# Kernel optimization log

Measured on AMD Instinct MI355X. Metric: run time of the kernel, lower is better.

Reference implementation:

```python
import jax, jax.numpy as jnp
import numpy as np

N_NODES = 100000
N_EDGES = 1600000
IN_G = 128
IN_R = 64
HID = 128
N_GRAPHS = 512
BN_EPS = 1e-5


def _gcn_conv(x, W, b, src, dst, norm, n_nodes):
    # PyG GCNConv: h = X W; out[i] = sum_j norm_ij * h[j] over edges (incl. self-loops); + bias
    h = x @ W  # [N, C]
    msgs = h[src] * norm[:, None]  # [E', C]
    agg = jax.ops.segment_sum(msgs, dst, num_segments=n_nodes)
    return agg + b


def setup_inputs() -> dict:
    key = jax.random.key(0)
    ks = jax.random.split(key, 12)
    x = jax.random.normal(ks[0], (N_NODES, IN_G), dtype=jnp.float32)
    edge_index = jax.random.randint(ks[1], (2, N_EDGES), 0, N_NODES, dtype=jnp.int64)
    batch = jnp.sort(jax.random.randint(ks[2], (N_NODES,), 0, N_GRAPHS, dtype=jnp.int64))
    rst = jax.random.normal(ks[3], (N_GRAPHS, IN_R), dtype=jnp.float32)

    def lin(k, fan_in, fan_out):
        bound = 1.0 / np.sqrt(fan_in)
        k1, k2 = jax.random.split(k)
        W = jax.random.uniform(k1, (fan_in, fan_out), minval=-bound, maxval=bound, dtype=jnp.float32)
        b = jax.random.uniform(k2, (fan_out,), minval=-bound, maxval=bound, dtype=jnp.float32)
        return W, b

    W1, b1 = lin(ks[4], IN_G, HID)
    W2, b2 = lin(ks[5], HID, HID)
    Wg, bg = lin(ks[6], HID, HID // 2)
    Wr, br = lin(ks[7], IN_R, HID // 2)
    Wc, bc = lin(ks[8], HID, 2)
    gamma = jnp.ones((HID,), dtype=jnp.float32)
    beta = jnp.zeros((HID,), dtype=jnp.float32)
    return {"x": x, "edge_index": edge_index, "batch": batch, "rst": rst,
            "num_graphs": N_GRAPHS,
            "W1": W1, "b1": b1, "gamma": gamma, "beta": beta,
            "W2": W2, "b2": b2, "Wg": Wg, "bg": bg,
            "Wr": Wr, "br": br, "Wc": Wc, "bc": bc}


def reference(x, edge_index, batch, rst, num_graphs,
              W1, b1, gamma, beta, W2, b2, Wg, bg, Wr, br, Wc, bc):
    n = x.shape[0]
    # add self-loops (PyG GCNConv default)
    loop = jnp.arange(n, dtype=edge_index.dtype)
    src = jnp.concatenate([edge_index[0], loop])
    dst = jnp.concatenate([edge_index[1], loop])
    deg = jax.ops.segment_sum(jnp.ones_like(dst, dtype=x.dtype), dst, num_segments=n)
    dinv = jnp.where(deg > 0, jax.lax.rsqrt(deg), 0.0)
    norm = dinv[src] * dinv[dst]  # [E+N]

    h = _gcn_conv(x, W1, b1, src, dst, norm, n)
    # BatchNorm1d with batch statistics (training math; dropout omitted / eval)
    mu = jnp.mean(h, axis=0)
    var = jnp.var(h, axis=0)
    h = gamma * (h - mu) * jax.lax.rsqrt(var + BN_EPS) + beta
    h = jax.nn.relu(h)
    h = _gcn_conv(h, W2, b2, src, dst, norm, n)

    # global mean pool
    sums = jax.ops.segment_sum(h, batch, num_segments=num_graphs)
    counts = jax.ops.segment_sum(jnp.ones((n,), dtype=h.dtype), batch, num_segments=num_graphs)
    pooled = sums / jnp.maximum(counts, 1.0)[:, None]  # [G, HID]

    x_graph = jax.nn.relu(pooled @ Wg + bg)
    x_rst = jax.nn.relu(rst @ Wr + br)
    x_comb = jnp.concatenate([x_graph, x_rst], axis=1)
    return x_comb @ Wc + bc
```

## Files before the change

kernel.cpp:

```cpp
#include <hip/hip_runtime.h>


typedef __attribute__((ext_vector_type(8))) short bf16x8;
typedef __attribute__((ext_vector_type(4))) float f32x4;
typedef __attribute__((ext_vector_type(2))) float f32x2;
typedef __attribute__((ext_vector_type(2))) unsigned u32x2;
typedef __attribute__((ext_vector_type(4))) unsigned u32x4;

#define NBKT_MAX 256
#define BKT_SHIFT 9
#define TILE_E 2000
#define BSORT_CAP 4096

__device__ __forceinline__ float bf_lo(unsigned u) {
  union { unsigned u; float f; } c; c.u = u << 16; return c.f;
}
__device__ __forceinline__ float bf_hi(unsigned u) {
  union { unsigned u; float f; } c; c.u = u & 0xffff0000u; return c.f;
}
__device__ __forceinline__ unsigned short f32_bf16(float f) {
  union { float f; unsigned u; } c; c.f = f;
  return (unsigned short)((c.u + 0x7fffu + ((c.u >> 16) & 1u)) >> 16);
}
__device__ __forceinline__ unsigned pack_bf16(float a, float b) {
  return (unsigned)f32_bf16(a) | ((unsigned)f32_bf16(b) << 16);
}
__device__ __forceinline__ unsigned pack_fp8x4(float c0, float c1, float c2, float c3) {
  int w = __builtin_amdgcn_cvt_pk_fp8_f32(c0, c1, 0, false);
  w = __builtin_amdgcn_cvt_pk_fp8_f32(c2, c3, w, true);
  return (unsigned)w;
}
__device__ __forceinline__ int aload(int* p) { return atomicAdd(p, 0); }

__global__ __launch_bounds__(256) void tile_hist_kernel(const int* __restrict__ dst,
                                                        int* __restrict__ tcnt,
                                                        int* __restrict__ counts,
                                                        float* __restrict__ stats,
                                                        const int* __restrict__ batch,
                                                        int* __restrict__ gstart,
                                                        int* __restrict__ syncp,
                                                        int e, int ntiles, int nbkt,
                                                        int n, int G) {
  __shared__ int hist[NBKT_MAX];
  int tile = blockIdx.x, tid = threadIdx.x;
  int idx = blockIdx.x * 256 + tid;
  if (idx < n) counts[idx] = 1;
  if (idx < 256) stats[idx] = 0.f;
  if (idx < 8) syncp[idx] = 0;
  if (idx <= G) {
    int g = idx;
    if (g == G) gstart[g] = n;
    else {
      int lo = 0, hi = n;
      while (lo < hi) {
        int mid = (lo + hi) >> 1;
        if (batch[mid] < g) lo = mid + 1; else hi = mid;
      }
      gstart[g] = lo;
    }
  }
  for (int b = tid; b < nbkt; b += 256) hist[b] = 0;
  __syncthreads();
  int t0 = tile * TILE_E;
  int tend = t0 + TILE_E; if (tend > e) tend = e;
  for (int i = t0 + tid; i < tend; i += 256)
    atomicAdd(&hist[__builtin_nontemporal_load(&dst[i]) >> BKT_SHIFT], 1);
  __syncthreads();
  for (int b = tid; b < nbkt; b += 256) tcnt[b * ntiles + tile] = hist[b];
}

__global__ __launch_bounds__(1024) void scan_ticket_kernel(const int* __restrict__ src,
                                                           int* __restrict__ dst,
                                                           int* __restrict__ bsum,
                                                           int* __restrict__ boff,
                                                           int* __restrict__ syncp,
                                                           float* __restrict__ dinv,
                                                           int n, int nb) {
  __shared__ int wsum[16];
  __shared__ int sflag, soff;
  int tid = threadIdx.x, lane = tid & 63, wid = tid >> 6;
  int bid = blockIdx.x;
  int idx = bid * 1024 + tid;
  int orig = (idx < n) ? src[idx] : 0;
  if (dinv != nullptr && idx < n) dinv[idx] = rsqrtf((float)orig);
  int v = orig;
#pragma unroll
  for (int d = 1; d < 64; d <<= 1) {
    int t = __shfl_up(v, d, 64);
    if (lane >= d) v += t;
  }
  if (lane == 63) wsum[wid] = v;
  __syncthreads();
  if (wid == 0 && lane < 16) {
    int s = wsum[lane];
#pragma unroll
    for (int d = 1; d < 16; d <<= 1) {
      int t = __shfl_up(s, d, 64);
      if (lane >= d) s += t;
    }
    wsum[lane] = s;
  }
  __syncthreads();
  int wexcl = (wid == 0) ? 0 : wsum[wid - 1];
  int lexcl = wexcl + (v - orig);
  if (tid == 0) {
    atomicExch(&bsum[bid], wsum[15]);
    __threadfence();
    int t = atomicAdd(&syncp[0], 1);
    sflag = (t == nb - 1) ? 1 : 0;
  }
  __syncthreads();
  if (sflag) {
    if (tid < 64) {
      int base = tid * 4;
      int a0 = (base + 0 < nb) ? aload(&bsum[base + 0]) : 0;
      int a1 = (base + 1 < nb) ? aload(&bsum[base + 1]) : 0;
      int a2 = (base + 2 < nb) ? aload(&bsum[base + 2]) : 0;
      int a3 = (base + 3 < nb) ? aload(&bsum[base + 3]) : 0;
      int local = a0 + a1 + a2 + a3, s = local;
#pragma unroll
      for (int d = 1; d < 64; d <<= 1) {
        int t = __shfl_up(s, d, 64);
        if (tid >= d) s += t;
      }
      int excl = s - local;
      if (base + 0 < nb) atomicExch(&boff[base + 0], excl);
      if (base + 1 < nb) atomicExch(&boff[base + 1], excl + a0);
      if (base + 2 < nb) atomicExch(&boff[base + 2], excl + a0 + a1);
      if (base + 3 < nb) atomicExch(&boff[base + 3], excl + a0 + a1 + a2);
      __threadfence();
    }
    __syncthreads();
    if (tid == 0) atomicExch(&syncp[1], 1);
  }
  if (tid == 0) {
    while (aload(&syncp[1]) == 0) __builtin_amdgcn_s_sleep(8);
    soff = aload(&boff[bid]);
  }
  __syncthreads();
  if (idx < n) dst[idx] = soff + lexcl;
}

__global__ __launch_bounds__(256) void tile_scatter_kernel(const int* __restrict__ src,
                                                           const int* __restrict__ dst,
                                                           const int* __restrict__ tcnt,
                                                           const int* __restrict__ toff,
                                                           int2* __restrict__ pedge,
                                                           int e, int ntiles, int nbkt) {
  __shared__ int hb[NBKT_MAX], cnt[NBKT_MAX], gbase[NBKT_MAX];
  __shared__ int2 led[TILE_E];
  int tile = blockIdx.x, tid = threadIdx.x;
  for (int b = tid; b < nbkt; b += 256) {
    hb[b] = tcnt[b * ntiles + tile];
    gbase[b] = toff[b * ntiles + tile];
    cnt[b] = 0;
  }
  __syncthreads();
  if (tid < 64) {
    int b4 = tid * 4;
    int h0 = (b4 + 0 < nbkt) ? hb[b4 + 0] : 0;
    int h1 = (b4 + 1 < nbkt) ? hb[b4 + 1] : 0;
    int h2 = (b4 + 2 < nbkt) ? hb[b4 + 2] : 0;
    int h3 = (b4 + 3 < nbkt) ? hb[b4 + 3] : 0;
    int local = h0 + h1 + h2 + h3, v = local;
#pragma unroll
    for (int d = 1; d < 64; d <<= 1) {
      int t = __shfl_up(v, d, 64);
      if (tid >= d) v += t;
    }
    int excl = v - local;
    if (b4 + 0 < nbkt) hb[b4 + 0] = excl;
    if (b4 + 1 < nbkt) hb[b4 + 1] = excl + h0;
    if (b4 + 2 < nbkt) hb[b4 + 2] = excl + h0 + h1;
    if (b4 + 3 < nbkt) hb[b4 + 3] = excl + h0 + h1 + h2;
  }
  __syncthreads();
  int t0 = tile * TILE_E;
  int tend = t0 + TILE_E; if (tend > e) tend = e;
  for (int i = t0 + tid; i < tend; i += 256) {
    int s = __builtin_nontemporal_load(&src[i]);
    int d = __builtin_nontemporal_load(&dst[i]);
    int bkt = d >> BKT_SHIFT;
    int slot = hb[bkt] + atomicAdd(&cnt[bkt], 1);
    led[slot] = make_int2(s, d);
  }
  __syncthreads();
  int tc = tend - t0;
  for (int j = tid; j < tc; j += 256) {
    int2 sd = led[j];
    int bkt = sd.y >> BKT_SHIFT;
    pedge[gbase[bkt] + (j - hb[bkt])] = sd;
  }
}

__global__ __launch_bounds__(256) void deg_count_kernel(const int2* __restrict__ pedge,
                                                        const int* __restrict__ toff,
                                                        int* __restrict__ counts,
                                                        int e, int ntiles, int nbkt, int n) {
  __shared__ int cnt[512];
  int b = blockIdx.x >> 2, qu = blockIdx.x & 3;
  int nb0 = b << BKT_SHIFT;
  int nn = n - nb0; if (nn > 512) nn = 512;
  for (int l = threadIdx.x; l < 512; l += 256) cnt[l] = 0;
  __syncthreads();
  int estart = toff[b * ntiles];
  int eend = (b + 1 < nbkt) ? toff[(b + 1) * ntiles] : e;
  int len = eend - estart;
  int qb = estart + (int)((long long)len * qu / 4);
  int qe = estart + (int)((long long)len * (qu + 1) / 4);
  for (int i = qb + threadIdx.x; i < qe; i += 256)
    atomicAdd(&cnt[pedge[i].y - nb0], 1);
  __syncthreads();
  for (int l = threadIdx.x; l < nn; l += 256) {
    int c = cnt[l];
    if (c) atomicAdd(&counts[nb0 + l], c);
  }
}

__global__ __launch_bounds__(256) void bucket_sort_kernel(const int2* __restrict__ pedge,
                                                          const int* __restrict__ toff,
                                                          const int* __restrict__ cursor,
                                                          int* __restrict__ sorted_src,
                                                          int e, int etot,
                                                          int ntiles, int nbkt, int n) {
  __shared__ int lcur[128];
  __shared__ int lsrc[BSORT_CAP];
  int b = blockIdx.x >> 2, qu = blockIdx.x & 3;
  int nb0 = b << BKT_SHIFT;
  int q0 = nb0 + qu * 128;
  if (q0 >= n) return;
  int q1 = q0 + 128; if (q1 > n) q1 = n;
  int qn = q1 - q0;
  int estart = toff[b * ntiles];
  int eend = (b + 1 < nbkt) ? toff[(b + 1) * ntiles] : e;
  int qstart = cursor[q0];
  int qend = (q1 < n) ? cursor[q1] : etot;
  for (int l = threadIdx.x; l < qn; l += 256) lcur[l] = cursor[q0 + l] - qstart;
  __syncthreads();
  for (int i = estart + threadIdx.x; i < eend; i += 256) {
    int2 sd = pedge[i];
    unsigned rel = (unsigned)(sd.y - q0);
    if (rel < (unsigned)qn) {
      int pos = atomicAdd(&lcur[rel], 1);
      if (pos < BSORT_CAP) lsrc[pos] = sd.x;
    }
  }
  __syncthreads();
  for (int l = threadIdx.x; l < qn; l += 256) {
    int pos = lcur[l];
    if (pos < BSORT_CAP) lsrc[pos] = q0 + l;
  }
  __syncthreads();
  int qc = qend - qstart; if (qc > BSORT_CAP) qc = BSORT_CAP;
  for (int j = threadIdx.x; j < qc; j += 256) sorted_src[qstart + j] = lsrc[j];
}

template <int MODE>
__global__ __launch_bounds__(256) void gemm_mfma_kernel(const void* __restrict__ Ap,
                                                        const float* __restrict__ W,
                                                        const float* __restrict__ dinv,
                                                        const float* __restrict__ stats,
                                                        const float* __restrict__ gamma,
                                                        const float* __restrict__ beta,
                                                        unsigned* __restrict__ Cb, int n) {
  __shared__ unsigned short WB[16384];
  __shared__ float scs[128], shs[128];
  int tid = threadIdx.x;
  if (MODE == 1 && tid < 128) {
    float invN = 1.f / (float)n;
    float mu = stats[tid] * invN;
    float var = stats[128 + tid] * invN - mu * mu;
    float rstd = rsqrtf(var + 1e-5f);
    float s = gamma[tid] * rstd;
    scs[tid] = s;
    shs[tid] = beta[tid] - mu * s;
  }
  for (int t = tid; t < 2048; t += 256) {
    int nl = t & 15, ct = (t >> 4) & 7, qq = (t >> 7) & 3, kt = t >> 9;
    int c = ct * 16 + nl;
    int k0 = kt * 32 + qq * 8;
    union { bf16x8 v; unsigned short s[8]; } u;
#pragma unroll
    for (int j = 0; j < 8; ++j) u.s[j] = f32_bf16(W[(k0 + j) * 128 + c]);
    *(bf16x8*)&WB[(size_t)t * 8] = u.v;
  }
  __syncthreads();
  int lane = tid & 63;
  int m = lane & 15, q = lane >> 4;
  float scr[4][8], shr[4][8];
  if (MODE == 1) {
#pragma unroll
    for (int kt = 0; kt < 4; ++kt)
#pragma unroll
      for (int j = 0; j < 8; ++j) {
        int c = kt * 32 + q * 8 + j;
        scr[kt][j] = scs[c];
        shr[kt][j] = shs[c];
      }
  }
  int wv = (int)((blockIdx.x * 256u + tid) >> 6);
  int nwv = (int)((gridDim.x * 256u) >> 6);
  int ntl = n >> 4;
  for (int t = wv; t < ntl; t += nwv) {
    int row = t * 16 + m;
    bf16x8 af[4];
    if (MODE == 1) {
      const u32x4* Au = (const u32x4*)((const unsigned*)Ap + (size_t)row * 64 + q * 4);
#pragma unroll
      for (int kt = 0; kt < 4; ++kt) {
        u32x4 w = Au[kt * 4];
        float y0 = fmaxf(fmaf(scr[kt][0], bf_lo(w.x), shr[kt][0]), 0.f);
        float y1 = fmaxf(fmaf(scr[kt][1], bf_hi(w.x), shr[kt][1]), 0.f);
        float y2 = fmaxf(fmaf(scr[kt][2], bf_lo(w.y), shr[kt][2]), 0.f);
        float y3 = fmaxf(fmaf(scr[kt][3], bf_hi(w.y), shr[kt][3]), 0.f);
        float y4 = fmaxf(fmaf(scr[kt][4], bf_lo(w.z), shr[kt][4]), 0.f);
        float y5 = fmaxf(fmaf(scr[kt][5], bf_hi(w.z), shr[kt][5]), 0.f);
        float y6 = fmaxf(fmaf(scr[kt][6], bf_lo(w.w), shr[kt][6]), 0.f);
        float y7 = fmaxf(fmaf(scr[kt][7], bf_hi(w.w), shr[kt][7]), 0.f);
        union { bf16x8 v; unsigned uu[4]; } uf;
        uf.uu[0] = pack_bf16(y0, y1);
        uf.uu[1] = pack_bf16(y2, y3);
        uf.uu[2] = pack_bf16(y4, y5);
        uf.uu[3] = pack_bf16(y6, y7);
        af[kt] = uf.v;
      }
    } else {
      const float* Arow = (const float*)Ap + (size_t)row * 128 + q * 8;
#pragma unroll
      for (int kt = 0; kt < 4; ++kt) {
        f32x4 a0 = *(const f32x4*)(Arow + kt * 32);
        f32x4 a1 = *(const f32x4*)(Arow + kt * 32 + 4);
        union { bf16x8 v; unsigned short s[8]; } u;
        u.s[0] = f32_bf16(a0.x); u.s[1] = f32_bf16(a0.y);
        u.s[2] = f32_bf16(a0.z); u.s[3] = f32_bf16(a0.w);
        u.s[4] = f32_bf16(a1.x); u.s[5] = f32_bf16(a1.y);
        u.s[6] = f32_bf16(a1.z); u.s[7] = f32_bf16(a1.w);
        af[kt] = u.v;
      }
    }
    f32x4 acc[8];
#pragma unroll
    for (int ct = 0; ct < 8; ++ct) acc[ct] = (f32x4){0.f, 0.f, 0.f, 0.f};
#pragma unroll
    for (int kt = 0; kt < 4; ++kt) {
#pragma unroll
      for (int ct = 0; ct < 8; ++ct) {
        bf16x8 b = *(const bf16x8*)&WB[(((kt * 4 + q) * 8 + ct) * 16 + m) * 8];
        acc[ct] = __builtin_amdgcn_mfma_f32_16x16x32_bf16(b, af[kt], acc[ct], 0, 0, 0);
      }
    }
    float dv = dinv[row];
#pragma unroll
    for (int ct = 0; ct < 8; ++ct) {
      unsigned wout = pack_fp8x4(acc[ct][0] * dv, acc[ct][1] * dv,
                                 acc[ct][2] * dv, acc[ct][3] * dv);
      Cb[(size_t)row * 32 + ct * 4 + q] = wout;
    }
  }
}

__global__ __launch_bounds__(256) void gather_kernel(const unsigned* __restrict__ g,
    const int* __restrict__ srcs, const int* __restrict__ cursor,
    const int* __restrict__ counts, const float* __restrict__ dinv,
    unsigned* __restrict__ out, int n) {
  int lane = threadIdx.x & 63;
  int grp = lane >> 4;
  int sub = lane & 15;
  int gw = (int)((blockIdx.x * blockDim.x + threadIdx.x) >> 6);
  int nw = (int)((gridDim.x * blockDim.x) >> 6);
  for (int i0 = gw; i0 < n; i0 += nw) {
    int i = __builtin_amdgcn_readfirstlane(i0);
    int beg = cursor[i];
    int cnt2 = counts[i];
    float di = dinv[i];
    f32x2 A0 = {0.f, 0.f}, A1 = {0.f, 0.f}, A2 = {0.f, 0.f}, A3 = {0.f, 0.f};
#define ACC8(W0, W1)                                                       \
    { A0 += __builtin_amdgcn_cvt_pk_f32_fp8((int)(W0), false);             \
      A1 += __builtin_amdgcn_cvt_pk_f32_fp8((int)(W0), true);              \
      A2 += __builtin_amdgcn_cvt_pk_f32_fp8((int)(W1), false);             \
      A3 += __builtin_amdgcn_cvt_pk_f32_fp8((int)(W1), true); }
    int e = 0;
    for (; e + 16 <= cnt2; e += 16) {
      int sA = srcs[beg + e + grp];
      int sB = srcs[beg + e + grp + 4];
      int sC = srcs[beg + e + grp + 8];
      int sD = srcs[beg + e + grp + 12];
      u32x2 vA = *((const u32x2*)(g + ((size_t)sA << 5)) + sub);
      u32x2 vB = *((const u32x2*)(g + ((size_t)sB << 5)) + sub);
      u32x2 vC = *((const u32x2*)(g + ((size_t)sC << 5)) + sub);
      u32x2 vD = *((const u32x2*)(g + ((size_t)sD << 5)) + sub);
      ACC8(vA.x, vA.y) ACC8(vB.x, vB.y) ACC8(vC.x, vC.y) ACC8(vD.x, vD.y)
    }
    for (; e + 4 <= cnt2; e += 4) {
      int s = srcs[beg + e + grp];
      u32x2 v = *((const u32x2*)(g + ((size_t)s << 5)) + sub);
      ACC8(v.x, v.y)
    }
    if (e < cnt2) {
      int k = e + grp;
      int kk = (k < cnt2) ? k : cnt2 - 1;
      int s = srcs[beg + kk];
      float sel = (k < cnt2) ? 1.f : 0.f;
      u32x2 v = *((const u32x2*)(g + ((size_t)s << 5)) + sub);
      f32x2 p0 = __builtin_amdgcn_cvt_pk_f32_fp8((int)v.x, false);
      f32x2 p1 = __builtin_amdgcn_cvt_pk_f32_fp8((int)v.x, true);
      f32x2 p2 = __builtin_amdgcn_cvt_pk_f32_fp8((int)v.y, false);
      f32x2 p3 = __builtin_amdgcn_cvt_pk_f32_fp8((int)v.y, true);
      A0 += p0 * sel; A1 += p1 * sel; A2 += p2 * sel; A3 += p3 * sel;
    }
#undef ACC8
    float a0 = A0.x, a1 = A0.y, a2 = A1.x, a3 = A1.y;
    float a4 = A2.x, a5 = A2.y, a6 = A3.x, a7 = A3.y;
    a0 += __shfl_xor(a0, 16, 64); a0 += __shfl_xor(a0, 32, 64);
    a1 += __shfl_xor(a1, 16, 64); a1 += __shfl_xor(a1, 32, 64);
    a2 += __shfl_xor(a2, 16, 64); a2 += __shfl_xor(a2, 32, 64);
    a3 += __shfl_xor(a3, 16, 64); a3 += __shfl_xor(a3, 32, 64);
    a4 += __shfl_xor(a4, 16, 64); a4 += __shfl_xor(a4, 32, 64);
    a5 += __shfl_xor(a5, 16, 64); a5 += __shfl_xor(a5, 32, 64);
    a6 += __shfl_xor(a6, 16, 64); a6 += __shfl_xor(a6, 32, 64);
    a7 += __shfl_xor(a7, 16, 64); a7 += __shfl_xor(a7, 32, 64);
    if (grp == 0) {
      u32x4 o;
      o.x = pack_bf16(di * a0, di * a1);
      o.y = pack_bf16(di * a2, di * a3);
      o.z = pack_bf16(di * a4, di * a5);
      o.w = pack_bf16(di * a6, di * a7);
      *((u32x4*)(out + ((size_t)i << 6)) + sub) = o;
    }
  }
}

__global__ __launch_bounds__(256) void bn_stats_kernel(const unsigned* __restrict__ a,
                                                       float* __restrict__ stats, int n) {
  int c2 = threadIdx.x & 63;
  int ph = threadIdx.x >> 6;
  float s0 = 0.f, s1 = 0.f, q0 = 0.f, q1 = 0.f;
  for (int r = blockIdx.x * 4 + ph; r < n; r += gridDim.x * 4) {
    unsigned v = a[(size_t)r * 64 + c2];
    float x0 = bf_lo(v), x1 = bf_hi(v);
    s0 += x0; s1 += x1; q0 += x0 * x0; q1 += x1 * x1;
  }
  __shared__ float ls[4][64][4];
  ls[ph][c2][0] = s0; ls[ph][c2][1] = s1; ls[ph][c2][2] = q0; ls[ph][c2][3] = q1;
  __syncthreads();
  if (threadIdx.x < 64) {
    int c = threadIdx.x;
    float S0 = 0.f, S1 = 0.f, Q0 = 0.f, Q1 = 0.f;
#pragma unroll
    for (int p = 0; p < 4; ++p) {
      S0 += ls[p][c][0]; S1 += ls[p][c][1]; Q0 += ls[p][c][2]; Q1 += ls[p][c][3];
    }
    atomicAdd(&stats[2 * c], S0);
    atomicAdd(&stats[2 * c + 1], S1);
    atomicAdd(&stats[128 + 2 * c], Q0);
    atomicAdd(&stats[129 + 2 * c], Q1);
  }
}

__global__ __launch_bounds__(256) void poolhead_kernel(const unsigned* __restrict__ a,
    const int* __restrict__ gstart, const float* __restrict__ b2,
    const float* __restrict__ rst, const float* __restrict__ Wg,
    const float* __restrict__ bg, const float* __restrict__ Wr,
    const float* __restrict__ br, const float* __restrict__ Wc,
    const float* __restrict__ bc, float* __restrict__ out, int G) {
  int g = blockIdx.x;
  int t = threadIdx.x;
  int c2 = t & 63;
  int ph = t >> 6;
  int s = gstart[g], e = gstart[g + 1];
  float a0 = 0.f, a1 = 0.f;
  for (int r = s + ph; r < e; r += 4) {
    unsigned v = a[(size_t)r * 64 + c2];
    a0 += bf_lo(v); a1 += bf_hi(v);
  }
  __shared__ float ls[4][64][2];
  __shared__ float xp[128];
  __shared__ float xc[128];
  ls[ph][c2][0] = a0; ls[ph][c2][1] = a1;
  __syncthreads();
  if (t < 64) {
    int c = t;
    float S0 = 0.f, S1 = 0.f;
#pragma unroll
    for (int p = 0; p < 4; ++p) { S0 += ls[p][c][0]; S1 += ls[p][c][1]; }
    int cnt = e - s;
    float inv = (cnt > 0) ? 1.f / (float)cnt : 0.f;
    xp[2 * c]     = (cnt > 0) ? (S0 * inv + b2[2 * c]) : 0.f;
    xp[2 * c + 1] = (cnt > 0) ? (S1 * inv + b2[2 * c + 1]) : 0.f;
  }
  __syncthreads();
  if (t < 64) {
    float acc = bg[t];
    for (int k = 0; k < 128; ++k) acc = fmaf(xp[k], Wg[k * 64 + t], acc);
    xc[t] = fmaxf(acc, 0.f);
  } else if (t < 128) {
    int j = t - 64;
    float acc = br[j];
    const float* __restrict__ r = rst + (size_t)g * 64;
    for (int k = 0; k < 64; ++k) acc = fmaf(r[k], Wr[k * 64 + j], acc);
    xc[t] = fmaxf(acc, 0.f);
  }
  __syncthreads();
  if (t < 2) {
    float acc = bc[t];
    for (int j = 0; j < 128; ++j) acc = fmaf(xc[j], Wc[j * 2 + t], acc);
    out[(size_t)g * 2 + t] = acc;
  }
}

extern "C" void kernel_launch(void* const* d_in, const int* in_sizes, int n_in,
                              void* d_out, int out_size, void* d_ws, size_t ws_size,
                              hipStream_t stream) {
  (void)n_in; (void)ws_size;
  const float* x     = (const float*)d_in[0];
  const int*   ei    = (const int*)d_in[1];
  const int*   batch = (const int*)d_in[2];
  const float* rst   = (const float*)d_in[3];
  const float* W1    = (const float*)d_in[5];
  const float* gamma = (const float*)d_in[7];
  const float* beta  = (const float*)d_in[8];
  const float* W2    = (const float*)d_in[9];
  const float* b2    = (const float*)d_in[10];
  const float* Wg    = (const float*)d_in[11];
  const float* bg    = (const float*)d_in[12];
  const float* Wr    = (const float*)d_in[13];
  const float* br    = (const float*)d_in[14];
  const float* Wc    = (const float*)d_in[15];
  const float* bc    = (const float*)d_in[16];
  float* out = (float*)d_out;

  int N = in_sizes[0] / 128;
  int E = in_sizes[1] / 2;
  int G = out_size / 2;
  int ETOT = E + N;
  const int* esrc = ei;
  const int* edst = ei + E;

  int nbkt = (N + 511) >> BKT_SHIFT;
  int ntiles = (E + TILE_E - 1) / TILE_E;
  int tlen = nbkt * ntiles;

  char* ws = (char*)d_ws;
  size_t off = 0;
  auto alloc = [&](size_t bytes) -> void* {
    void* p = ws + off;
    off += (bytes + 255) & ~(size_t)255;
    return p;
  };
  unsigned* hb  = (unsigned*)alloc((size_t)N * 32 * 4);
  unsigned* agb = (unsigned*)alloc((size_t)N * 64 * 4);
  int* sorted   = (int*)alloc((size_t)ETOT * 4 + 256);
  int2* pedge   = (int2*)alloc((size_t)E * 8);
  int* tcnt     = (int*)alloc((size_t)tlen * 4);
  int* toff     = (int*)alloc((size_t)tlen * 4);
  int* counts   = (int*)alloc((size_t)N * 4);
  int* cursor   = (int*)alloc((size_t)N * 4);
  float* dinv   = (float*)alloc((size_t)N * 4);
  float* stats  = (float*)alloc(256 * 4);
  int* gstart   = (int*)alloc((size_t)(G + 1) * 4);
  int* bsum     = (int*)alloc(256 * 4);
  int* boff     = (int*)alloc(256 * 4);
  int* syncp    = (int*)alloc(8 * 4);

  int nscan = (N + 1023) / 1024;
  int ntscan = (tlen + 1023) / 1024;
  int gblocks = (N / 16 + 3) / 4;

  tile_hist_kernel<<<ntiles, 256, 0, stream>>>(edst, tcnt, counts, stats, batch,
                                               gstart, syncp, E, ntiles, nbkt, N, G);
  scan_ticket_kernel<<<ntscan, 1024, 0, stream>>>(tcnt, toff, bsum, boff,
                                                  syncp, nullptr, tlen, ntscan);
  tile_scatter_kernel<<<ntiles, 256, 0, stream>>>(esrc, edst, tcnt, toff, pedge, E, ntiles, nbkt);
  deg_count_kernel<<<nbkt * 4, 256, 0, stream>>>(pedge, toff, counts, E, ntiles, nbkt, N);
  scan_ticket_kernel<<<nscan, 1024, 0, stream>>>(counts, cursor, bsum, boff,
                                                 syncp + 2, dinv, N, nscan);
  bucket_sort_kernel<<<nbkt * 4, 256, 0, stream>>>(pedge, toff, cursor, sorted,
                                                   E, ETOT, ntiles, nbkt, N);

  gemm_mfma_kernel<0><<<gblocks, 256, 0, stream>>>(x, W1, dinv, stats, gamma, beta, hb, N);
  gather_kernel<<<4096, 256, 0, stream>>>(hb, sorted, cursor, counts, dinv, agb, N);

  bn_stats_kernel<<<512, 256, 0, stream>>>(agb, stats, N);

  gemm_mfma_kernel<1><<<gblocks, 256, 0, stream>>>(agb, W2, dinv, stats, gamma, beta, hb, N);
  gather_kernel<<<4096, 256, 0, stream>>>(hb, sorted, cursor, counts, dinv, agb, N);

  poolhead_kernel<<<G, 256, 0, stream>>>(agb, gstart, b2, rst, Wg, bg, Wr, br,
                                         Wc, bc, out, G);
}
```

Measured before the change: 375.6 us.

## Fold degree counting into scatter and prefetch next tile in GEMM

```diff
diff --git a/kernel.cpp b/kernel.cpp
--- a/kernel.cpp
+++ b/kernel.cpp
@@ -44,7 +44,7 @@
   __shared__ int hist[NBKT_MAX];
   int tile = blockIdx.x, tid = threadIdx.x;
   int idx = blockIdx.x * 256 + tid;
-  if (idx < n) counts[idx] = 1;
+  if (idx < n) counts[idx] = 0;
   if (idx < 256) stats[idx] = 0.f;
   if (idx < 8) syncp[idx] = 0;
   if (idx <= G) {
@@ -75,13 +75,13 @@
                                                            int* __restrict__ boff,
                                                            int* __restrict__ syncp,
                                                            float* __restrict__ dinv,
-                                                           int n, int nb) {
+                                                           int n, int nb, int addone) {
   __shared__ int wsum[16];
   __shared__ int sflag, soff;
   int tid = threadIdx.x, lane = tid & 63, wid = tid >> 6;
   int bid = blockIdx.x;
   int idx = bid * 1024 + tid;
-  int orig = (idx < n) ? src[idx] : 0;
+  int orig = (idx < n) ? (src[idx] + addone) : 0;
   if (dinv != nullptr && idx < n) dinv[idx] = rsqrtf((float)orig);
   int v = orig;
 #pragma unroll
@@ -146,6 +146,7 @@
                                                            const int* __restrict__ tcnt,
                                                            const int* __restrict__ toff,
                                                            int2* __restrict__ pedge,
+                                                           int* __restrict__ counts,
                                                            int e, int ntiles, int nbkt) {
   __shared__ int hb[NBKT_MAX], cnt[NBKT_MAX], gbase[NBKT_MAX];
   __shared__ int2 led[TILE_E];
@@ -183,6 +184,7 @@
     int bkt = d >> BKT_SHIFT;
     int slot = hb[bkt] + atomicAdd(&cnt[bkt], 1);
     led[slot] = make_int2(s, d);
+    atomicAdd(&counts[d], 1);
   }
   __syncthreads();
   int tc = tend - t0;
@@ -190,30 +192,6 @@
     int2 sd = led[j];
     int bkt = sd.y >> BKT_SHIFT;
     pedge[gbase[bkt] + (j - hb[bkt])] = sd;
-  }
-}
-
-__global__ __launch_bounds__(256) void deg_count_kernel(const int2* __restrict__ pedge,
-                                                        const int* __restrict__ toff,
-                                                        int* __restrict__ counts,
-                                                        int e, int ntiles, int nbkt, int n) {
-  __shared__ int cnt[512];
-  int b = blockIdx.x >> 2, qu = blockIdx.x & 3;
-  int nb0 = b << BKT_SHIFT;
-  int nn = n - nb0; if (nn > 512) nn = 512;
-  for (int l = threadIdx.x; l < 512; l += 256) cnt[l] = 0;
-  __syncthreads();
-  int estart = toff[b * ntiles];
-  int eend = (b + 1 < nbkt) ? toff[(b + 1) * ntiles] : e;
-  int len = eend - estart;
-  int qb = estart + (int)((long long)len * qu / 4);
-  int qe = estart + (int)((long long)len * (qu + 1) / 4);
-  for (int i = qb + threadIdx.x; i < qe; i += 256)
-    atomicAdd(&cnt[pedge[i].y - nb0], 1);
-  __syncthreads();
-  for (int l = threadIdx.x; l < nn; l += 256) {
-    int c = cnt[l];
-    if (c) atomicAdd(&counts[nb0 + l], c);
   }
 }
 
@@ -301,14 +279,45 @@
   int wv = (int)((blockIdx.x * 256u + tid) >> 6);
   int nwv = (int)((gridDim.x * 256u) >> 6);
   int ntl = n >> 4;
+  if (wv >= ntl) return;
+  f32x4 cf0, cf1, cf2, cf3, cf4, cf5, cf6, cf7;
+  u32x4 cu0, cu1, cu2, cu3;
+  {
+    int row = wv * 16 + m;
+    if (MODE == 1) {
+      const u32x4* Au = (const u32x4*)((const unsigned*)Ap + (size_t)row * 64 + q * 4);
+      cu0 = Au[0]; cu1 = Au[4]; cu2 = Au[8]; cu3 = Au[12];
+    } else {
+      const float* Ar = (const float*)Ap + (size_t)row * 128 + q * 8;
+      cf0 = *(const f32x4*)(Ar);       cf1 = *(const f32x4*)(Ar + 4);
+      cf2 = *(const f32x4*)(Ar + 32);  cf3 = *(const f32x4*)(Ar + 36);
+      cf4 = *(const f32x4*)(Ar + 64);  cf5 = *(const f32x4*)(Ar + 68);
+      cf6 = *(const f32x4*)(Ar + 96);  cf7 = *(const f32x4*)(Ar + 100);
+    }
+  }
   for (int t = wv; t < ntl; t += nwv) {
-    int row = t * 16 + m;
+    int tn = t + nwv;
+    f32x4 nf0, nf1, nf2, nf3, nf4, nf5, nf6, nf7;
+    u32x4 nu0, nu1, nu2, nu3;
+    if (tn < ntl) {
+      int row = tn * 16 + m;
+      if (MODE == 1) {
+        const u32x4* Au = (const u32x4*)((const unsigned*)Ap + (size_t)row * 64 + q * 4);
+        nu0 = Au[0]; nu1 = Au[4]; nu2 = Au[8]; nu3 = Au[12];
+      } else {
+        const float* Ar = (const float*)Ap + (size_t)row * 128 + q * 8;
+        nf0 = *(const f32x4*)(Ar);       nf1 = *(const f32x4*)(Ar + 4);
+        nf2 = *(const f32x4*)(Ar + 32);  nf3 = *(const f32x4*)(Ar + 36);
+        nf4 = *(const f32x4*)(Ar + 64);  nf5 = *(const f32x4*)(Ar + 68);
+        nf6 = *(const f32x4*)(Ar + 96);  nf7 = *(const f32x4*)(Ar + 100);
+      }
+    }
     bf16x8 af[4];
     if (MODE == 1) {
-      const u32x4* Au = (const u32x4*)((const unsigned*)Ap + (size_t)row * 64 + q * 4);
+      u32x4 ww[4] = {cu0, cu1, cu2, cu3};
 #pragma unroll
       for (int kt = 0; kt < 4; ++kt) {
-        u32x4 w = Au[kt * 4];
+        u32x4 w = ww[kt];
         float y0 = fmaxf(fmaf(scr[kt][0], bf_lo(w.x), shr[kt][0]), 0.f);
         float y1 = fmaxf(fmaf(scr[kt][1], bf_hi(w.x), shr[kt][1]), 0.f);
         float y2 = fmaxf(fmaf(scr[kt][2], bf_lo(w.y), shr[kt][2]), 0.f);
@@ -325,11 +334,11 @@
         af[kt] = uf.v;
       }
     } else {
-      const float* Arow = (const float*)Ap + (size_t)row * 128 + q * 8;
+      f32x4 lo[4] = {cf0, cf2, cf4, cf6};
+      f32x4 hi[4] = {cf1, cf3, cf5, cf7};
 #pragma unroll
       for (int kt = 0; kt < 4; ++kt) {
-        f32x4 a0 = *(const f32x4*)(Arow + kt * 32);
-        f32x4 a1 = *(const f32x4*)(Arow + kt * 32 + 4);
+        f32x4 a0 = lo[kt], a1 = hi[kt];
         union { bf16x8 v; unsigned short s[8]; } u;
         u.s[0] = f32_bf16(a0.x); u.s[1] = f32_bf16(a0.y);
         u.s[2] = f32_bf16(a0.z); u.s[3] = f32_bf16(a0.w);
@@ -349,6 +358,7 @@
         acc[ct] = __builtin_amdgcn_mfma_f32_16x16x32_bf16(b, af[kt], acc[ct], 0, 0, 0);
       }
     }
+    int row = t * 16 + m;
     float dv = dinv[row];
 #pragma unroll
     for (int ct = 0; ct < 8; ++ct) {
@@ -356,6 +366,9 @@
                                  acc[ct][2] * dv, acc[ct][3] * dv);
       Cb[(size_t)row * 32 + ct * 4 + q] = wout;
     }
+    if (MODE == 1) { cu0 = nu0; cu1 = nu1; cu2 = nu2; cu3 = nu3; }
+    else { cf0 = nf0; cf1 = nf1; cf2 = nf2; cf3 = nf3;
+           cf4 = nf4; cf5 = nf5; cf6 = nf6; cf7 = nf7; }
   }
 }
 
@@ -371,7 +384,7 @@
   for (int i0 = gw; i0 < n; i0 += nw) {
     int i = __builtin_amdgcn_readfirstlane(i0);
     int beg = cursor[i];
-    int cnt2 = counts[i];
+    int cnt2 = counts[i] + 1;
     float di = dinv[i];
     f32x2 A0 = {0.f, 0.f}, A1 = {0.f, 0.f}, A2 = {0.f, 0.f}, A3 = {0.f, 0.f};
 #define ACC8(W0, W1)                                                       \
@@ -564,16 +577,16 @@
 
   int nscan = (N + 1023) / 1024;
   int ntscan = (tlen + 1023) / 1024;
-  int gblocks = (N / 16 + 3) / 4;
+  int gblocks = (N / 16 + 15) / 16;
 
   tile_hist_kernel<<<ntiles, 256, 0, stream>>>(edst, tcnt, counts, stats, batch,
                                                gstart, syncp, E, ntiles, nbkt, N, G);
   scan_ticket_kernel<<<ntscan, 1024, 0, stream>>>(tcnt, toff, bsum, boff,
-                                                  syncp, nullptr, tlen, ntscan);
-  tile_scatter_kernel<<<ntiles, 256, 0, stream>>>(esrc, edst, tcnt, toff, pedge, E, ntiles, nbkt);
-  deg_count_kernel<<<nbkt * 4, 256, 0, stream>>>(pedge, toff, counts, E, ntiles, nbkt, N);
+                                                  syncp, nullptr, tlen, ntscan, 0);
+  tile_scatter_kernel<<<ntiles, 256, 0, stream>>>(esrc, edst, tcnt, toff, pedge,
+                                                  counts, E, ntiles, nbkt);
   scan_ticket_kernel<<<nscan, 1024, 0, stream>>>(counts, cursor, bsum, boff,
-                                                 syncp + 2, dinv, N, nscan);
+                                                 syncp + 2, dinv, N, nscan, 1);
   bucket_sort_kernel<<<nbkt * 4, 256, 0, stream>>>(pedge, toff, cursor, sorted,
                                                    E, ETOT, ntiles, nbkt, N);
 
```

After: 419.8 us. 11.8% more time.
